# Kernel tuning notes

Measured on AMD Instinct MI355X. Metric: run time of the kernel, lower is better.

## Reference

```python
import jax, jax.numpy as jnp
import numpy as np

N_NODES = 100000
NODE_FEATS = 8  # len(graph_node_feature_dict) - 1


def gcn_conv(h, W, b, src, dst, deg_inv_sqrt):
    """PyG GCNConv: h @ W, symmetric-normalized aggregation with self-loops, + bias."""
    n = h.shape[0]
    hw = h @ W  # [N, out]
    norm = (deg_inv_sqrt[src] * deg_inv_sqrt[dst])[:, None]  # [E, 1]
    agg = jax.ops.segment_sum(hw[src] * norm, dst, num_segments=n)
    # self-loop contribution: norm_ii = deg_i^{-1}
    agg = agg + hw * (deg_inv_sqrt ** 2)[:, None]
    return agg + b


def setup_inputs() -> dict:
    key = jax.random.key(0)
    ks = jax.random.split(key, 16)
    N, E = N_NODES, 800000
    in_dim, hid, out_dim, n_hidden_layers = 16, 128, 3, 4
    x = jax.random.normal(ks[0], (N, 10), dtype=jnp.float32)
    x_mask = jax.random.uniform(ks[1], (N, 10), dtype=jnp.float32)
    edge_index = jax.random.randint(ks[2], (2, E), 0, N, dtype=jnp.int32)
    s = 0.05
    W0 = jax.random.normal(ks[3], (in_dim, hid), dtype=jnp.float32) * s
    b0 = jnp.zeros((hid,), dtype=jnp.float32)
    Wh = jax.random.normal(ks[4], (n_hidden_layers, hid, hid), dtype=jnp.float32) * s
    bh = jnp.zeros((n_hidden_layers, hid), dtype=jnp.float32)
    Wr1 = jax.random.normal(ks[5], (hid, hid), dtype=jnp.float32) * s
    br1 = jnp.zeros((hid,), dtype=jnp.float32)
    Wr2 = jax.random.normal(ks[6], (hid, out_dim), dtype=jnp.float32) * s
    br2 = jnp.zeros((out_dim,), dtype=jnp.float32)
    return dict(x=x, x_mask=x_mask, edge_index=edge_index, W0=W0, b0=b0,
                Wh=Wh, bh=bh, Wr1=Wr1, br1=br1, Wr2=Wr2, br2=br2)


def reference(x, x_mask, edge_index, W0, b0, Wh, bh, Wr1, br1, Wr2, br2):
    N = x.shape[0]
    src, dst = edge_index[0], edge_index[1]
    # degree over (A + I), counted at aggregation target (PyG gcn_norm uses col)
    deg = jax.ops.segment_sum(jnp.ones(src.shape[0], dtype=x.dtype), dst,
                              num_segments=N) + 1.0
    deg_inv_sqrt = jax.lax.rsqrt(deg)

    h = jnp.concatenate([x[:, :NODE_FEATS], x_mask[:, :NODE_FEATS]], axis=1)
    h = gcn_conv(h, W0, b0, src, dst, deg_inv_sqrt)
    emb = h
    h = jax.nn.relu(h)
    for i in range(Wh.shape[0]):
        h = gcn_conv(h, Wh[i], bh[i], src, dst, deg_inv_sqrt)
        emb = h
        h = jax.nn.relu(h)
    pred = jax.nn.relu(h @ Wr1 + br1) @ Wr2 + br2
    return (emb, pred)
```

## Files before the change

kernel.cpp:

```cpp
#include <hip/hip_runtime.h>
#include <cstdint>
#include <cstddef>

typedef __attribute__((ext_vector_type(8))) short short8;
typedef __attribute__((ext_vector_type(4))) float f32x4;
typedef __attribute__((ext_vector_type(4))) _Float16 half4v;
typedef __attribute__((ext_vector_type(2))) _Float16 half2v;


__device__ inline unsigned short f2bf(float f) {
    unsigned int u = __float_as_uint(f);
    u = u + 0x7fff + ((u >> 16) & 1);
    return (unsigned short)(u >> 16);
}
__device__ inline float bf2f(unsigned short h) {
    return __uint_as_float(((unsigned int)h) << 16);
}
__device__ inline void split2(float v, unsigned short& hi, unsigned short& lo) {
    hi = f2bf(v);
    lo = f2bf(v - bf2f(hi));
}

__device__ __forceinline__ half2v ld_h2(const _Float16* p, unsigned off) {
    return *(const half2v*)((const char*)p + off);
}
__device__ __forceinline__ float ld_f(const float* p, unsigned off) {
    return *(const float*)((const char*)p + off);
}


__global__ void zero_ints(int* p, int n) {
    int i = blockIdx.x * 256 + threadIdx.x;
    if (i < n) p[i] = 0;
}

__global__ void count_deg(const int* __restrict__ dst, int* __restrict__ cnt, int E) {
    int i = blockIdx.x * 256 + threadIdx.x;
    if (i < E) atomicAdd(&cnt[dst[i]], 1);
}

__global__ void compute_dis(const int* __restrict__ cnt, float* __restrict__ dis, int N) {
    int i = blockIdx.x * 256 + threadIdx.x;
    if (i < N) dis[i] = rsqrtf((float)cnt[i] + 1.0f);
}


__global__ __launch_bounds__(256) void scan_block_sums(const int* __restrict__ cnt,
                                                       int* __restrict__ partials, int N) {
    __shared__ int s[256];
    int t = threadIdx.x;
    int base = blockIdx.x * 1024 + t * 4;
    int v = 0;
    if (base + 3 < N) {
        int4 d = *(const int4*)&cnt[base];
        v = d.x + d.y + d.z + d.w;
    } else {
        for (int j = 0; j < 4; ++j) if (base + j < N) v += cnt[base + j];
    }
    s[t] = v;
    __syncthreads();
    for (int off = 128; off > 0; off >>= 1) {
        if (t < off) s[t] += s[t + off];
        __syncthreads();
    }
    if (t == 0) partials[blockIdx.x] = s[0];
}

__global__ __launch_bounds__(256) void scan_partials(int* __restrict__ partials, int nb,
                                                     int* __restrict__ rp, int N) {
    __shared__ int s[256];
    int t = threadIdx.x;
    int base = t * 4;
    int v0 = 0, v1 = 0, v2 = 0, v3 = 0;
    if (base < nb)     v0 = partials[base];
    if (base + 1 < nb) v1 = partials[base + 1];
    if (base + 2 < nb) v2 = partials[base + 2];
    if (base + 3 < nb) v3 = partials[base + 3];
    s[t] = v0 + v1 + v2 + v3;
    __syncthreads();
    for (int off = 1; off < 256; off <<= 1) {
        int v = s[t];
        int u = (t >= off) ? s[t - off] : 0;
        __syncthreads();
        s[t] = v + u;
        __syncthreads();
    }
    int run = (t == 0) ? 0 : s[t - 1];
    if (base < nb)     { partials[base] = run;     run += v0; }
    if (base + 1 < nb) { partials[base + 1] = run; run += v1; }
    if (base + 2 < nb) { partials[base + 2] = run; run += v2; }
    if (base + 3 < nb) { partials[base + 3] = run; run += v3; }
    if (t == 255) rp[N] = s[255];
}

__global__ __launch_bounds__(256) void scan_write(const int* __restrict__ cnt,
                                                  const int* __restrict__ partials,
                                                  int* __restrict__ rp,
                                                  int* __restrict__ cursor, int N) {
    __shared__ int s[256];
    int t = threadIdx.x;
    int base = blockIdx.x * 1024 + t * 4;
    int v0 = 0, v1 = 0, v2 = 0, v3 = 0;
    if (base + 3 < N) {
        int4 d = *(const int4*)&cnt[base];
        v0 = d.x; v1 = d.y; v2 = d.z; v3 = d.w;
    } else {
        if (base < N)     v0 = cnt[base];
        if (base + 1 < N) v1 = cnt[base + 1];
        if (base + 2 < N) v2 = cnt[base + 2];
    }
    s[t] = v0 + v1 + v2 + v3;
    __syncthreads();
    for (int off = 1; off < 256; off <<= 1) {
        int v = s[t];
        int u = (t >= off) ? s[t - off] : 0;
        __syncthreads();
        s[t] = v + u;
        __syncthreads();
    }
    int run = partials[blockIdx.x] + ((t == 0) ? 0 : s[t - 1]);
    int4 o;
    o.x = run; run += v0;
    o.y = run; run += v1;
    o.z = run; run += v2;
    o.w = run; run += v3;
    if (base + 3 < N) {
        *(int4*)&rp[base] = o;
        *(int4*)&cursor[base] = o;
    } else {
        if (base < N)     { rp[base] = o.x;     cursor[base] = o.x; }
        if (base + 1 < N) { rp[base + 1] = o.y; cursor[base + 1] = o.y; }
        if (base + 2 < N) { rp[base + 2] = o.z; cursor[base + 2] = o.z; }
    }
}

__global__ void scatter_edges(const int* __restrict__ src, const int* __restrict__ dstv,
                              const float* __restrict__ dis, int* __restrict__ cursor,
                              int2* __restrict__ edata, int E) {
    int i = blockIdx.x * 256 + threadIdx.x;
    if (i < E) {
        int s = src[i], d = dstv[i];
        int pos = atomicAdd(&cursor[d], 1);
        edata[pos] = make_int2(s, __float_as_int(dis[s] * dis[d]));
    }
}

__global__ void build_h0(const float* __restrict__ x, const float* __restrict__ xm,
                         float* __restrict__ h0, int N) {
    int i = blockIdx.x * 256 + threadIdx.x;
    if (i < N * 16) {
        int node = i >> 4, f = i & 15;
        h0[i] = (f < 8) ? x[node * 10 + f] : xm[node * 10 + f - 8];
    }
}


__global__ __launch_bounds__(256) void wsplit_kernel(const float* __restrict__ Wh,
                                                     const float* __restrict__ Wr1,
                                                     unsigned short* __restrict__ whi,
                                                     unsigned short* __restrict__ wlo) {
    int g = blockIdx.x * 256 + threadIdx.x;
    int l = g >> 14;
    int idx = g & 16383;
    int j = idx & 7;
    int lane = (idx >> 3) & 63;
    int tcchunk = idx >> 9;
    int tc = tcchunk & 7, chunk = tcchunk >> 3;
    int k = chunk * 32 + (lane >> 4) * 8 + j;
    int n = tc * 16 + (lane & 15);
    float v = (l < 4) ? Wh[l * 16384 + k * 128 + n] : Wr1[k * 128 + n];
    unsigned short hi, lo;
    split2(v, hi, lo);
    whi[g] = hi;
    wlo[g] = lo;
}


__device__ __forceinline__ float agg_node_l0(
    const float* __restrict__ h0, const int2* __restrict__ edata,
    const float* __restrict__ dis,
    int node, int beg, int deg, int es, int f, int N) {
    float acc = 0.f;
    if (node < N) {
        float di = dis[node];
        float sf = ld_f(h0, ((unsigned)node << 6) + (f << 2));
        acc = (es == 0) ? sf * (di * di) : 0.f;
        const int2* ep = edata + beg;
        if (deg > 0 && deg <= 8) {
            int2 rec[8];
            #pragma unroll
            for (int j = 0; j < 8; ++j) rec[j] = ep[j];
            int ixs = rec[0].x;
            float vv[2], nn[2];
            #pragma unroll
            for (int b = 0; b < 2; ++b) {
                int x0 = rec[b * 4 + 0].x, x1 = rec[b * 4 + 1].x;
                int x2 = rec[b * 4 + 2].x, x3 = rec[b * 4 + 3].x;
                int y0 = rec[b * 4 + 0].y, y1 = rec[b * 4 + 1].y;
                int y2 = rec[b * 4 + 2].y, y3 = rec[b * 4 + 3].y;
                int ix = (es == 0) ? x0 : (es == 1) ? x1 : (es == 2) ? x2 : x3;
                int iy = (es == 0) ? y0 : (es == 1) ? y1 : (es == 2) ? y2 : y3;
                int j = b * 4 + es;
                ix = (j < deg) ? ix : ixs;
                vv[b] = ld_f(h0, ((unsigned)ix << 6) + (f << 2));
                nn[b] = (j < deg) ? __int_as_float(iy) : 0.f;
            }
            acc += nn[0] * vv[0];
            acc += nn[1] * vv[1];
        } else if (deg > 8) {
            for (int eb = 0; eb < deg; eb += 16) {
                int2 rec[16];
                #pragma unroll
                for (int j = 0; j < 16; ++j) rec[j] = ep[eb + j];
                int c = min(deg - eb, 16);
                int ixs = rec[0].x;
                float vv[4], nn[4];
                #pragma unroll
                for (int b = 0; b < 4; ++b) {
                    int x0 = rec[b * 4 + 0].x, x1 = rec[b * 4 + 1].x;
                    int x2 = rec[b * 4 + 2].x, x3 = rec[b * 4 + 3].x;
                    int y0 = rec[b * 4 + 0].y, y1 = rec[b * 4 + 1].y;
                    int y2 = rec[b * 4 + 2].y, y3 = rec[b * 4 + 3].y;
                    int ix = (es == 0) ? x0 : (es == 1) ? x1 : (es == 2) ? x2 : x3;
                    int iy = (es == 0) ? y0 : (es == 1) ? y1 : (es == 2) ? y2 : y3;
                    int j = b * 4 + es;
                    ix = (j < c) ? ix : ixs;
                    vv[b] = ld_f(h0, ((unsigned)ix << 6) + (f << 2));
                    nn[b] = (j < c) ? __int_as_float(iy) : 0.f;
                }
                #pragma unroll
                for (int b = 0; b < 4; ++b) acc += nn[b] * vv[b];
            }
        }
    }
    acc += __shfl_xor(acc, 16);
    acc += __shfl_xor(acc, 32);
    return acc;
}

__device__ __forceinline__ void store_row_hidden(unsigned short* sAh, unsigned short* sAl,
                                                 int r, int ln, float a0, float a1) {
    unsigned short h0_, l0_, h1_, l1_;
    split2(a0, h0_, l0_);
    split2(a1, h1_, l1_);
    int bo = (r * 256 + ln * 4) ^ ((r & 7) << 4);
    ushort2 hh; hh.x = h0_; hh.y = h1_;
    ushort2 ll; ll.x = l0_; ll.y = l1_;
    *(ushort2*)((char*)sAh + bo) = hh;
    *(ushort2*)((char*)sAl + bo) = ll;
}

__device__ __forceinline__ void agg_node_hidden(
    const _Float16* __restrict__ hin, const int2* __restrict__ edata,
    const float* __restrict__ dis,
    int node, int beg, int deg, int ln, int N,
    unsigned short* sAh, unsigned short* sAl, int r) {
    float a0 = 0.f, a1 = 0.f;
    if (node < N) {
        float di = dis[node];
        float sc = di * di;
        unsigned lb = (unsigned)(ln << 2);
        half2v sv = ld_h2(hin, ((unsigned)node << 8) + lb);
        a0 = (float)sv[0] * sc;
        a1 = (float)sv[1] * sc;
        const int2* ep = edata + beg;
        if (deg > 0 && deg <= 8) {
            int2 rec[8];
            #pragma unroll
            for (int j = 0; j < 8; ++j) rec[j] = ep[j];
            int ix0 = rec[0].x;
            half2v va[8];
            #pragma unroll
            for (int j = 0; j < 8; ++j) {
                int ix = (j < deg) ? rec[j].x : ix0;
                va[j] = ld_h2(hin, ((unsigned)ix << 8) + lb);
            }
            #pragma unroll
            for (int j = 0; j < 8; ++j) {
                float nr = (j < deg) ? __int_as_float(rec[j].y) : 0.f;
                a0 += nr * (float)va[j][0];
                a1 += nr * (float)va[j][1];
            }
        } else if (deg > 8) {
            int2 rec[16];
            #pragma unroll
            for (int j = 0; j < 16; ++j) rec[j] = ep[j];
            int c = min(deg, 16);
            int ix0 = rec[0].x;
            half2v va[16];
            #pragma unroll
            for (int j = 0; j < 16; ++j) {
                int ix = (j < c) ? rec[j].x : ix0;
                va[j] = ld_h2(hin, ((unsigned)ix << 8) + lb);
            }
            #pragma unroll
            for (int j = 0; j < 16; ++j) {
                float nr = (j < c) ? __int_as_float(rec[j].y) : 0.f;
                a0 += nr * (float)va[j][0];
                a1 += nr * (float)va[j][1];
            }
            for (int e = 16; e < deg; ++e) {
                int2 rr2 = ep[e];
                half2v v = ld_h2(hin, ((unsigned)rr2.x << 8) + lb);
                float nr = __int_as_float(rr2.y);
                a0 += nr * (float)v[0];
                a1 += nr * (float)v[1];
            }
        }
    }
    store_row_hidden(sAh, sAl, r, ln, a0, a1);
}


__global__ __launch_bounds__(256, 8) void fused_layer0_kernel(
    const float* __restrict__ h0,
    const int* __restrict__ rp, const int2* __restrict__ edata,
    const float* __restrict__ dis,
    const float* __restrict__ W0, const float* __restrict__ b0,
    _Float16* __restrict__ hout, int N) {
    __shared__ float sA[32][17];
    __shared__ float sW[2048];
    int t = threadIdx.x;
    int node0 = blockIdx.x * 32;
    for (int i = t * 4; i < 2048; i += 1024)
        *(float4*)&sW[i] = *(const float4*)&W0[i];

    {
        int wv = __builtin_amdgcn_readfirstlane(t >> 6);
        int ln = t & 63;
        int es = ln >> 4, f = ln & 15;
        int base = node0 + wv * 8;
        int rr[9];
        #pragma unroll
        for (int i = 0; i < 9; ++i) rr[i] = rp[min(base + i, N)];
        #pragma unroll
        for (int it = 0; it < 8; ++it) {
            float acc = agg_node_l0(h0, edata, dis, base + it, rr[it],
                                    rr[it + 1] - rr[it], es, f, N);
            if (es == 0) sA[wv * 8 + it][f] = acc;
        }
    }
    __syncthreads();

    int r2 = t >> 3;
    int c0 = (t & 7) * 16;
    float a16[16];
    #pragma unroll
    for (int c = 0; c < 16; ++c) a16[c] = 0.f;
    #pragma unroll
    for (int k = 0; k < 16; ++k) {
        float a = sA[r2][k];
        #pragma unroll
        for (int c = 0; c < 16; ++c) a16[c] += a * sW[k * 128 + c0 + c];
    }
    int row = node0 + r2;
    if (row < N) {
        #pragma unroll
        for (int cc = 0; cc < 16; cc += 4) {
            half4v o;
            #pragma unroll
            for (int u = 0; u < 4; ++u)
                o[u] = (_Float16)fmaxf(a16[cc + u] + b0[c0 + cc + u], 0.f);
            *(half4v*)&hout[(size_t)row * 128 + c0 + cc] = o;
        }
    }
}


template <bool LAST>
__global__ __launch_bounds__(256, 8) void fused_layer_kernel(
    const _Float16* __restrict__ hin,
    const int* __restrict__ rp, const int2* __restrict__ edata,
    const float* __restrict__ dis,
    const unsigned short* __restrict__ whi, const unsigned short* __restrict__ wlo,
    const float* __restrict__ bias,
    void* __restrict__ outv,
    const unsigned short* __restrict__ w1hi, const unsigned short* __restrict__ w1lo,
    const float* __restrict__ br1, const float* __restrict__ Wr2,
    const float* __restrict__ br2, float* __restrict__ pred,
    int N) {
    __shared__ unsigned short sAh[4096];
    __shared__ unsigned short sAl[4096];
    int t = threadIdx.x;
    int node0 = blockIdx.x * 32;

    {
        int wv1 = __builtin_amdgcn_readfirstlane(t >> 6);
        int ln = t & 63;
        int base = node0 + wv1 * 8;
        int rr[9];
        #pragma unroll
        for (int i = 0; i < 9; ++i) rr[i] = rp[min(base + i, N)];
        #pragma unroll
        for (int it = 0; it < 8; ++it)
            agg_node_hidden(hin, edata, dis, base + it, rr[it],
                            rr[it + 1] - rr[it], ln, N, sAh, sAl, wv1 * 8 + it);
    }
    __syncthreads();

    int wv = t >> 6, ln2 = t & 63;
    int m = ln2 & 15, q = ln2 >> 4;
    int rg = wv & 1, ch = wv >> 1;
    int rloc = rg * 16 + m;
    int tcb = ch * 4;

    f32x4 acc[4];
    #pragma unroll
    for (int i = 0; i < 4; ++i) acc[i] = (f32x4)(0.f);

    #pragma unroll
    for (int chunk = 0; chunk < 4; ++chunk) {
        int bo = (rloc * 256 + q * 16 + chunk * 64) ^ ((rloc & 7) << 4);
        short8 af = *(const short8*)((const char*)sAh + bo);
        short8 lf = *(const short8*)((const char*)sAl + bo);
        const unsigned short* wb = whi + (size_t)(chunk * 8 + tcb) * 512 + ln2 * 8;
        const unsigned short* wc = wlo + (size_t)(chunk * 8 + tcb) * 512 + ln2 * 8;
        #pragma unroll
        for (int j = 0; j < 4; ++j) {
            short8 wh = *(const short8*)(wb + j * 512);
            short8 wl = *(const short8*)(wc + j * 512);
            acc[j] = __builtin_amdgcn_mfma_f32_16x16x32_bf16(af, wh, acc[j], 0, 0, 0);
            acc[j] = __builtin_amdgcn_mfma_f32_16x16x32_bf16(lf, wh, acc[j], 0, 0, 0);
            acc[j] = __builtin_amdgcn_mfma_f32_16x16x32_bf16(af, wl, acc[j], 0, 0, 0);
        }
    }

    int crow = node0 + rg * 16 + q * 4;

    if constexpr (!LAST) {
        _Float16* hout = (_Float16*)outv;
        #pragma unroll
        for (int j = 0; j < 4; ++j) {
            int col = (tcb + j) * 16 + m;
            float b = bias[col];
            #pragma unroll
            for (int r = 0; r < 4; ++r) {
                int rr = crow + r;
                if (rr < N) {
                    float v = fmaxf(acc[j][r] + b, 0.f);
                    hout[(size_t)rr * 128 + col] = (_Float16)v;
                }
            }
        }
    } else {
        __shared__ float pbuf[2][16][3];
        float* emb = (float*)outv;
        #pragma unroll
        for (int j = 0; j < 4; ++j) {
            int col = (tcb + j) * 16 + m;
            float b = bias[col];
            #pragma unroll
            for (int r = 0; r < 4; ++r) {
                int rr = crow + r;
                if (rr < N)
                    __builtin_nontemporal_store(acc[j][r] + b, &emb[(size_t)rr * 128 + col]);
            }
        }
        __syncthreads();
        #pragma unroll
        for (int j = 0; j < 4; ++j) {
            int col = (tcb + j) * 16 + m;
            float b = bias[col];
            #pragma unroll
            for (int r = 0; r < 4; ++r) {
                int r2 = rg * 16 + q * 4 + r;
                float v = fmaxf(acc[j][r] + b, 0.f);
                unsigned short hi, lo;
                split2(v, hi, lo);
                int bo = (r2 * 256 + col * 2) ^ ((r2 & 7) << 4);
                *(unsigned short*)((char*)sAh + bo) = hi;
                *(unsigned short*)((char*)sAl + bo) = lo;
            }
        }
        __syncthreads();
        f32x4 acc2[4];
        #pragma unroll
        for (int i = 0; i < 4; ++i) acc2[i] = (f32x4)(0.f);
        #pragma unroll
        for (int chunk = 0; chunk < 4; ++chunk) {
            int bo = (rloc * 256 + q * 16 + chunk * 64) ^ ((rloc & 7) << 4);
            short8 af = *(const short8*)((const char*)sAh + bo);
            short8 lf = *(const short8*)((const char*)sAl + bo);
            const unsigned short* wb = w1hi + (size_t)(chunk * 8 + tcb) * 512 + ln2 * 8;
            const unsigned short* wc = w1lo + (size_t)(chunk * 8 + tcb) * 512 + ln2 * 8;
            #pragma unroll
            for (int j = 0; j < 4; ++j) {
                short8 wh = *(const short8*)(wb + j * 512);
                short8 wl = *(const short8*)(wc + j * 512);
                acc2[j] = __builtin_amdgcn_mfma_f32_16x16x32_bf16(af, wh, acc2[j], 0, 0, 0);
                acc2[j] = __builtin_amdgcn_mfma_f32_16x16x32_bf16(lf, wh, acc2[j], 0, 0, 0);
                acc2[j] = __builtin_amdgcn_mfma_f32_16x16x32_bf16(af, wl, acc2[j], 0, 0, 0);
            }
        }
        float p0[4] = {0.f, 0.f, 0.f, 0.f};
        float p1[4] = {0.f, 0.f, 0.f, 0.f};
        float p2[4] = {0.f, 0.f, 0.f, 0.f};
        #pragma unroll
        for (int j = 0; j < 4; ++j) {
            int col = (tcb + j) * 16 + m;
            float b1 = br1[col];
            float w0 = Wr2[col * 3 + 0], w1 = Wr2[col * 3 + 1], w2 = Wr2[col * 3 + 2];
            #pragma unroll
            for (int r = 0; r < 4; ++r) {
                float hv = fmaxf(acc2[j][r] + b1, 0.f);
                p0[r] += hv * w0;
                p1[r] += hv * w1;
                p2[r] += hv * w2;
            }
        }
        #pragma unroll
        for (int mask = 1; mask < 16; mask <<= 1) {
            #pragma unroll
            for (int r = 0; r < 4; ++r) {
                p0[r] += __shfl_xor(p0[r], mask);
                p1[r] += __shfl_xor(p1[r], mask);
                p2[r] += __shfl_xor(p2[r], mask);
            }
        }
        if (ch == 1 && m == 0) {
            #pragma unroll
            for (int r = 0; r < 4; ++r) {
                pbuf[rg][q * 4 + r][0] = p0[r];
                pbuf[rg][q * 4 + r][1] = p1[r];
                pbuf[rg][q * 4 + r][2] = p2[r];
            }
        }
        __syncthreads();
        if (ch == 0 && m == 0) {
            #pragma unroll
            for (int r = 0; r < 4; ++r) {
                int rr = crow + r;
                if (rr < N) {
                    float o0 = p0[r] + pbuf[rg][q * 4 + r][0] + br2[0];
                    float o1 = p1[r] + pbuf[rg][q * 4 + r][1] + br2[1];
                    float o2 = p2[r] + pbuf[rg][q * 4 + r][2] + br2[2];
                    __builtin_nontemporal_store(o0, &pred[(size_t)rr * 3 + 0]);
                    __builtin_nontemporal_store(o1, &pred[(size_t)rr * 3 + 1]);
                    __builtin_nontemporal_store(o2, &pred[(size_t)rr * 3 + 2]);
                }
            }
        }
    }
}


extern "C" void kernel_launch(void* const* d_in, const int* in_sizes, int n_in,
                              void* d_out, int out_size, void* d_ws, size_t ws_size,
                              hipStream_t stream) {
    const float* x   = (const float*)d_in[0];
    const float* xm  = (const float*)d_in[1];
    const int*   ei  = (const int*)d_in[2];
    const float* W0  = (const float*)d_in[3];
    const float* b0  = (const float*)d_in[4];
    const float* Wh  = (const float*)d_in[5];
    const float* bh  = (const float*)d_in[6];
    const float* Wr1 = (const float*)d_in[7];
    const float* br1 = (const float*)d_in[8];
    const float* Wr2 = (const float*)d_in[9];
    const float* br2 = (const float*)d_in[10];
    float* out = (float*)d_out;

    int N = in_sizes[0] / 10;
    int E = in_sizes[2] / 2;
    const int* src = ei;
    const int* dst = ei + E;

    float* emb_out  = out;
    float* pred_out = out + (size_t)N * 128;

    char* ws = (char*)d_ws;
    size_t off = 0;
    auto alloc = [&](size_t bytes) -> void* {
        void* p = ws + off;
        off += (bytes + 255) & ~(size_t)255;
        return p;
    };
    _Float16* bufA = (_Float16*)alloc((size_t)N * 128 * 2);
    _Float16* bufB = (_Float16*)alloc((size_t)N * 128 * 2);
    float* h0       = (float*)bufB;
    int*   cnt      = (int*)alloc((size_t)N * 4);
    float* dis      = (float*)alloc((size_t)N * 4);
    int*   rp       = (int*)alloc((size_t)(N + 1) * 4);
    int*   cursor   = (int*)alloc((size_t)N * 4);
    int2*  edata    = (int2*)alloc((size_t)E * 8);
    int*   partials = (int*)alloc((size_t)1024 * 4);
    unsigned short* whi = (unsigned short*)alloc((size_t)5 * 16384 * 2);
    unsigned short* wlo = (unsigned short*)alloc((size_t)5 * 16384 * 2);
    (void)ws_size;

    int gN = (N + 255) / 256, gE = (E + 255) / 256;
    int gRows32 = (N + 31) / 32;
    int nScanBlocks = (N + 1023) / 1024;

    zero_ints<<<gN, 256, 0, stream>>>(cnt, N);
    count_deg<<<gE, 256, 0, stream>>>(dst, cnt, E);
    compute_dis<<<gN, 256, 0, stream>>>(cnt, dis, N);
    scan_block_sums<<<nScanBlocks, 256, 0, stream>>>(cnt, partials, N);
    scan_partials<<<1, 256, 0, stream>>>(partials, nScanBlocks, rp, N);
    scan_write<<<nScanBlocks, 256, 0, stream>>>(cnt, partials, rp, cursor, N);
    scatter_edges<<<gE, 256, 0, stream>>>(src, dst, dis, cursor, edata, E);
    build_h0<<<(N * 16 + 255) / 256, 256, 0, stream>>>(x, xm, h0, N);
    wsplit_kernel<<<5 * 16384 / 256, 256, 0, stream>>>(Wh, Wr1, whi, wlo);

    fused_layer0_kernel<<<gRows32, 256, 0, stream>>>(h0, rp, edata, dis, W0, b0, bufA, N);

    fused_layer_kernel<false><<<gRows32, 256, 0, stream>>>(
        bufA, rp, edata, dis, whi, wlo, bh, bufB,
        nullptr, nullptr, nullptr, nullptr, nullptr, nullptr, N);
    fused_layer_kernel<false><<<gRows32, 256, 0, stream>>>(
        bufB, rp, edata, dis, whi + 16384, wlo + 16384, bh + 128, bufA,
        nullptr, nullptr, nullptr, nullptr, nullptr, nullptr, N);
    fused_layer_kernel<false><<<gRows32, 256, 0, stream>>>(
        bufA, rp, edata, dis, whi + 2 * 16384, wlo + 2 * 16384, bh + 2 * 128, bufB,
        nullptr, nullptr, nullptr, nullptr, nullptr, nullptr, N);
    fused_layer_kernel<true><<<gRows32, 256, 0, stream>>>(
        bufB, rp, edata, dis, whi + 3 * 16384, wlo + 3 * 16384, bh + 3 * 128, emb_out,
        whi + 4 * 16384, wlo + 4 * 16384, br1, Wr2, br2, pred_out, N);
}
```

Measured before the change: 469.8 us.

## Fuse degree normalization into scan and read raw inputs directly in layer 0

```diff
diff --git a/kernel.cpp b/kernel.cpp
--- a/kernel.cpp
+++ b/kernel.cpp
@@ -37,11 +37,6 @@
 __global__ void count_deg(const int* __restrict__ dst, int* __restrict__ cnt, int E) {
     int i = blockIdx.x * 256 + threadIdx.x;
     if (i < E) atomicAdd(&cnt[dst[i]], 1);
-}
-
-__global__ void compute_dis(const int* __restrict__ cnt, float* __restrict__ dis, int N) {
-    int i = blockIdx.x * 256 + threadIdx.x;
-    if (i < N) dis[i] = rsqrtf((float)cnt[i] + 1.0f);
 }
 
 
@@ -96,7 +91,8 @@
 __global__ __launch_bounds__(256) void scan_write(const int* __restrict__ cnt,
                                                   const int* __restrict__ partials,
                                                   int* __restrict__ rp,
-                                                  int* __restrict__ cursor, int N) {
+                                                  int* __restrict__ cursor,
+                                                  float* __restrict__ dis, int N) {
     __shared__ int s[256];
     int t = threadIdx.x;
     int base = blockIdx.x * 1024 + t * 4;
@@ -127,10 +123,16 @@
     if (base + 3 < N) {
         *(int4*)&rp[base] = o;
         *(int4*)&cursor[base] = o;
+        float4 dv;
+        dv.x = rsqrtf((float)v0 + 1.0f);
+        dv.y = rsqrtf((float)v1 + 1.0f);
+        dv.z = rsqrtf((float)v2 + 1.0f);
+        dv.w = rsqrtf((float)v3 + 1.0f);
+        *(float4*)&dis[base] = dv;
     } else {
-        if (base < N)     { rp[base] = o.x;     cursor[base] = o.x; }
-        if (base + 1 < N) { rp[base + 1] = o.y; cursor[base + 1] = o.y; }
-        if (base + 2 < N) { rp[base + 2] = o.z; cursor[base + 2] = o.z; }
+        if (base < N)     { rp[base] = o.x;     cursor[base] = o.x; dis[base] = rsqrtf((float)v0 + 1.0f); }
+        if (base + 1 < N) { rp[base + 1] = o.y; cursor[base + 1] = o.y; dis[base + 1] = rsqrtf((float)v1 + 1.0f); }
+        if (base + 2 < N) { rp[base + 2] = o.z; cursor[base + 2] = o.z; dis[base + 2] = rsqrtf((float)v2 + 1.0f); }
     }
 }
 
@@ -142,15 +144,6 @@
         int s = src[i], d = dstv[i];
         int pos = atomicAdd(&cursor[d], 1);
         edata[pos] = make_int2(s, __float_as_int(dis[s] * dis[d]));
-    }
-}
-
-__global__ void build_h0(const float* __restrict__ x, const float* __restrict__ xm,
-                         float* __restrict__ h0, int N) {
-    int i = blockIdx.x * 256 + threadIdx.x;
-    if (i < N * 16) {
-        int node = i >> 4, f = i & 15;
-        h0[i] = (f < 8) ? x[node * 10 + f] : xm[node * 10 + f - 8];
     }
 }
 
@@ -176,14 +169,16 @@
 }
 
 
+
 __device__ __forceinline__ float agg_node_l0(
-    const float* __restrict__ h0, const int2* __restrict__ edata,
-    const float* __restrict__ dis,
+    const float* __restrict__ x, const float* __restrict__ xm,
+    const int2* __restrict__ edata, const float* __restrict__ dis,
     int node, int beg, int deg, int es, int f, int N) {
+    const float* psel = (f < 8) ? (x + f) : (xm + (f - 8));
     float acc = 0.f;
     if (node < N) {
         float di = dis[node];
-        float sf = ld_f(h0, ((unsigned)node << 6) + (f << 2));
+        float sf = ld_f(psel, (unsigned)node * 40u);
         acc = (es == 0) ? sf * (di * di) : 0.f;
         const int2* ep = edata + beg;
         if (deg > 0 && deg <= 8) {
@@ -202,7 +197,7 @@
                 int iy = (es == 0) ? y0 : (es == 1) ? y1 : (es == 2) ? y2 : y3;
                 int j = b * 4 + es;
                 ix = (j < deg) ? ix : ixs;
-                vv[b] = ld_f(h0, ((unsigned)ix << 6) + (f << 2));
+                vv[b] = ld_f(psel, (unsigned)ix * 40u);
                 nn[b] = (j < deg) ? __int_as_float(iy) : 0.f;
             }
             acc += nn[0] * vv[0];
@@ -225,7 +220,7 @@
                     int iy = (es == 0) ? y0 : (es == 1) ? y1 : (es == 2) ? y2 : y3;
                     int j = b * 4 + es;
                     ix = (j < c) ? ix : ixs;
-                    vv[b] = ld_f(h0, ((unsigned)ix << 6) + (f << 2));
+                    vv[b] = ld_f(psel, (unsigned)ix * 40u);
                     nn[b] = (j < c) ? __int_as_float(iy) : 0.f;
                 }
                 #pragma unroll
@@ -313,7 +308,7 @@
 
 
 __global__ __launch_bounds__(256, 8) void fused_layer0_kernel(
-    const float* __restrict__ h0,
+    const float* __restrict__ x, const float* __restrict__ xm,
     const int* __restrict__ rp, const int2* __restrict__ edata,
     const float* __restrict__ dis,
     const float* __restrict__ W0, const float* __restrict__ b0,
@@ -335,33 +330,41 @@
         for (int i = 0; i < 9; ++i) rr[i] = rp[min(base + i, N)];
         #pragma unroll
         for (int it = 0; it < 8; ++it) {
-            float acc = agg_node_l0(h0, edata, dis, base + it, rr[it],
+            float acc = agg_node_l0(x, xm, edata, dis, base + it, rr[it],
                                     rr[it + 1] - rr[it], es, f, N);
             if (es == 0) sA[wv * 8 + it][f] = acc;
         }
     }
     __syncthreads();
 
-    int r2 = t >> 3;
-    int c0 = (t & 7) * 16;
-    float a16[16];
+    int cg = t & 31, rg2 = t >> 5;
+    int c0 = cg * 4;
+    float4 acc4[4];
     #pragma unroll
-    for (int c = 0; c < 16; ++c) a16[c] = 0.f;
+    for (int i = 0; i < 4; ++i) acc4[i] = make_float4(0.f, 0.f, 0.f, 0.f);
     #pragma unroll
     for (int k = 0; k < 16; ++k) {
-        float a = sA[r2][k];
-        #pragma unroll
-        for (int c = 0; c < 16; ++c) a16[c] += a * sW[k * 128 + c0 + c];
-    }
-    int row = node0 + r2;
-    if (row < N) {
-        #pragma unroll
-        for (int cc = 0; cc < 16; cc += 4) {
+        float4 w = *(const float4*)&sW[k * 128 + c0];
+        #pragma unroll
+        for (int i = 0; i < 4; ++i) {
+            float a = sA[rg2 * 4 + i][k];
+            acc4[i].x += a * w.x;
+            acc4[i].y += a * w.y;
+            acc4[i].z += a * w.z;
+            acc4[i].w += a * w.w;
+        }
+    }
+    float4 bb = *(const float4*)&b0[c0];
+    #pragma unroll
+    for (int i = 0; i < 4; ++i) {
+        int row = node0 + rg2 * 4 + i;
+        if (row < N) {
             half4v o;
-            #pragma unroll
-            for (int u = 0; u < 4; ++u)
-                o[u] = (_Float16)fmaxf(a16[cc + u] + b0[c0 + cc + u], 0.f);
-            *(half4v*)&hout[(size_t)row * 128 + c0 + cc] = o;
+            o[0] = (_Float16)fmaxf(acc4[i].x + bb.x, 0.f);
+            o[1] = (_Float16)fmaxf(acc4[i].y + bb.y, 0.f);
+            o[2] = (_Float16)fmaxf(acc4[i].z + bb.z, 0.f);
+            o[3] = (_Float16)fmaxf(acc4[i].w + bb.w, 0.f);
+            *(half4v*)&hout[(size_t)row * 128 + c0] = o;
         }
     }
 }
@@ -577,7 +580,6 @@
     };
     _Float16* bufA = (_Float16*)alloc((size_t)N * 128 * 2);
     _Float16* bufB = (_Float16*)alloc((size_t)N * 128 * 2);
-    float* h0       = (float*)bufB;
     int*   cnt      = (int*)alloc((size_t)N * 4);
     float* dis      = (float*)alloc((size_t)N * 4);
     int*   rp       = (int*)alloc((size_t)(N + 1) * 4);
@@ -594,15 +596,13 @@
 
     zero_ints<<<gN, 256, 0, stream>>>(cnt, N);
     count_deg<<<gE, 256, 0, stream>>>(dst, cnt, E);
-    compute_dis<<<gN, 256, 0, stream>>>(cnt, dis, N);
     scan_block_sums<<<nScanBlocks, 256, 0, stream>>>(cnt, partials, N);
     scan_partials<<<1, 256, 0, stream>>>(partials, nScanBlocks, rp, N);
-    scan_write<<<nScanBlocks, 256, 0, stream>>>(cnt, partials, rp, cursor, N);
+    scan_write<<<nScanBlocks, 256, 0, stream>>>(cnt, partials, rp, cursor, dis, N);
     scatter_edges<<<gE, 256, 0, stream>>>(src, dst, dis, cursor, edata, E);
-    build_h0<<<(N * 16 + 255) / 256, 256, 0, stream>>>(x, xm, h0, N);
     wsplit_kernel<<<5 * 16384 / 256, 256, 0, stream>>>(Wh, Wr1, whi, wlo);
 
-    fused_layer0_kernel<<<gRows32, 256, 0, stream>>>(h0, rp, edata, dis, W0, b0, bufA, N);
+    fused_layer0_kernel<<<gRows32, 256, 0, stream>>>(x, xm, rp, edata, dis, W0, b0, bufA, N);
 
     fused_layer_kernel<false><<<gRows32, 256, 0, stream>>>(
         bufA, rp, edata, dis, whi, wlo, bh, bufB,
```

Result: slower. 683.7 us (+45.5%).
